# Optimization experiments

Hardware: AMD Instinct MI355X
Metric: run time of the kernel (lower is better)

The kernel has to match this reference:

```python
import jax, jax.numpy as jnp
import numpy as np

B, T, I, H, O = 65536, 28, 28, 64, 10


def setup_inputs() -> dict:
    key = jax.random.key(0)
    ks = jax.random.split(key, 8)
    s = 1.0 / np.sqrt(H)
    return {
        "x": jax.random.normal(ks[0], (B, T, I), dtype=jnp.float32),
        # PyTorch LSTM params: gate order i, f, g, o stacked along first dim
        "W_ih": jax.random.uniform(ks[1], (4 * H, I), minval=-s, maxval=s, dtype=jnp.float32),
        "W_hh": jax.random.uniform(ks[2], (4 * H, H), minval=-s, maxval=s, dtype=jnp.float32),
        "b_ih": jax.random.uniform(ks[3], (4 * H,), minval=-s, maxval=s, dtype=jnp.float32),
        "b_hh": jax.random.uniform(ks[4], (4 * H,), minval=-s, maxval=s, dtype=jnp.float32),
        "W_out": jax.random.uniform(ks[5], (O, H), minval=-s, maxval=s, dtype=jnp.float32),
        "b_out": jax.random.uniform(ks[6], (O,), minval=-s, maxval=s, dtype=jnp.float32),
    }


def _lstm_last_h(x, W_ih, W_hh, b_ih, b_hh):
    # x: [B, T, I]; returns final hidden state h_T: [B, H]
    b = b_ih + b_hh
    # precompute input projections for all timesteps: [T, B, 4H]
    xg = jnp.einsum("bti,gi->tbg", x, W_ih) + b

    def step(carry, xg_t):
        h, c = carry
        gates = xg_t + h @ W_hh.T  # [B, 4H]
        i, f, g, o = jnp.split(gates, 4, axis=-1)
        i = jax.nn.sigmoid(i)
        f = jax.nn.sigmoid(f)
        g = jnp.tanh(g)
        o = jax.nn.sigmoid(o)
        c = f * c + i * g
        h = o * jnp.tanh(c)
        return (h, c), None

    h0 = jnp.zeros((x.shape[0], W_hh.shape[1]), dtype=x.dtype)
    (h, c), _ = jax.lax.scan(step, (h0, h0), xg)
    return h


def reference(x, W_ih, W_hh, b_ih, b_hh, W_out, b_out):
    h = _lstm_last_h(x, W_ih, W_hh, b_ih, b_hh)  # [B, H]
    return h @ W_out.T + b_out  # [B, O]
```

## Files before the change

### kernel.cpp

```cpp
#include <hip/hip_runtime.h>
#include <hip/hip_bf16.h>
#include <stdint.h>
#include <stddef.h>

#define T_STEPS 28
#define I_DIM 28
#define H_DIM 64
#define O_DIM 10
#define BT 32
#define NTHREADS 256

typedef short bf16x8  __attribute__((ext_vector_type(8)));
typedef float f32x4   __attribute__((ext_vector_type(4)));

#define KS (-1.4426950408889634f)
#define KG ( 2.8853900817779268f)

__device__ __forceinline__ short f2bf(float f){
    uint32_t u = __builtin_bit_cast(uint32_t, f);
    u = (u + 0x7fffu + ((u >> 16) & 1u)) >> 16;
    return (short)u;
}
__device__ __forceinline__ float bf2f(short v){
    return __builtin_bit_cast(float, (uint32_t)(uint16_t)v << 16);
}
__device__ __forceinline__ uint32_t pack_bf16x2(float lo, float hi){
    float2 p2; p2.x = lo; p2.y = hi;
    __hip_bfloat162 p = __float22bfloat162_rn(p2);
    uint32_t u;
    __builtin_memcpy(&u, &p, 4);
    return u;
}

#define X_OFF(b)  ((b) * 2560)
#define H_OFF(b)  (5120 + (b) * 4608)
#define SMEM_BYTES (16896 + 48)

__global__ __launch_bounds__(NTHREADS, 4)
void lstm_fused(const float* __restrict__ x,
                const float* __restrict__ W_ih,
                const float* __restrict__ W_hh,
                const float* __restrict__ b_ih,
                const float* __restrict__ b_hh,
                const float* __restrict__ W_out,
                const float* __restrict__ b_out,
                float* __restrict__ out)
{
    __shared__ alignas(16) unsigned char smem[SMEM_BYTES];
    float* wout_t = (float*)(smem + 14336);
    float* bout_s = (float*)(smem + 16896);

    const int tid    = threadIdx.x;
    const int w      = tid >> 6;
    const int jgroup = w;
    const int lane = tid & 63;
    const int col  = lane & 15;
    const int quad = lane >> 4;
    const int jcol = jgroup * 16 + col;
    const int b0   = blockIdx.x * BT;

    bf16x8 wih[4];
    bf16x8 whh[2][4];
    #pragma unroll
    for (int nt = 0; nt < 4; ++nt){
        const float sc = (nt == 2) ? KG : KS;
        const int n = nt * 64 + jgroup * 16 + col;
        #pragma unroll
        for (int j = 0; j < 8; ++j){
            const int k = quad * 8 + j;
            wih[nt][j] = (k < I_DIM) ? f2bf(sc * W_ih[n * I_DIM + k])
                       : (k == I_DIM) ? f2bf(sc * (b_ih[n] + b_hh[n]))
                       : (short)0;
        }
        #pragma unroll
        for (int s = 0; s < 2; ++s)
            #pragma unroll
            for (int j = 0; j < 8; ++j){
                const int k = s * 32 + quad * 8 + j;
                whh[s][nt][j] = f2bf(sc * W_hh[n * H_DIM + k]);
            }
    }
    const f32x4 z4 = {0.0f, 0.0f, 0.0f, 0.0f};

    for (int idx = tid; idx < H_DIM * O_DIM; idx += NTHREADS){
        const int j = idx / O_DIM;
        const int o = idx - j * O_DIM;
        wout_t[idx] = W_out[o * H_DIM + j];
    }
    if (tid < O_DIM) bout_s[tid] = b_out[tid];

    for (int idx = tid; idx < BT * 72; idx += NTHREADS)
        ((short*)(smem + H_OFF(0)))[idx] = 0;

    const int row = tid >> 3;
    const int seg = tid & 7;
    const float* pxs = x + (size_t)(b0 + row) * (T_STEPS * I_DIM) + seg * 4;

    float xa[4];
    #pragma unroll
    for (int u = 0; u < 4; ++u){
        const int c = seg * 4 + u;
        xa[u] = (c < I_DIM) ? pxs[u] : (c == I_DIM ? 1.0f : 0.0f);
    }
    pxs += I_DIM;

    float cst[2][4];
    #pragma unroll
    for (int m = 0; m < 2; ++m)
        #pragma unroll
        for (int r = 0; r < 4; ++r) cst[m][r] = 0.0f;

    for (int t = 0; t < T_STEPS; ++t){
        short (*xb)[40] = (short(*)[40])(smem + X_OFF(t & 1));
        {
            uint2 v;
            v.x = pack_bf16x2(xa[0], xa[1]);
            v.y = pack_bf16x2(xa[2], xa[3]);
            *(uint2*)&xb[row][seg * 4] = v;
        }
        __syncthreads();

        if (t < T_STEPS - 1){
            #pragma unroll
            for (int u = 0; u < 4; ++u)
                if (seg * 4 + u < I_DIM) xa[u] = pxs[u];
            pxs += I_DIM;
        }

        const short (*hr)[72] = (const short(*)[72])(smem + H_OFF(t & 1));
        short (*hw)[72]       = (short(*)[72])(smem + H_OFF((t + 1) & 1));

        #pragma unroll
        for (int m = 0; m < 2; ++m){
            const int mt = m;

            f32x4 acc[4];
            {
                bf16x8 a = *(const bf16x8*)&xb[mt * 16 + col][quad * 8];
                #pragma unroll
                for (int nt = 0; nt < 4; ++nt)
                    acc[nt] = __builtin_amdgcn_mfma_f32_16x16x32_bf16(a, wih[nt], z4, 0, 0, 0);
            }
            #pragma unroll
            for (int s = 0; s < 2; ++s){
                bf16x8 a = *(const bf16x8*)&hr[mt * 16 + col][s * 32 + quad * 8];
                #pragma unroll
                for (int nt = 0; nt < 4; ++nt)
                    acc[nt] = __builtin_amdgcn_mfma_f32_16x16x32_bf16(a, whh[s][nt], acc[nt], 0, 0, 0);
            }

            float hv[4];
            #pragma unroll
            for (int p = 0; p < 2; ++p){
                const int r0 = 2 * p, r1 = 2 * p + 1;
                const float dA0 = 1.0f + __builtin_amdgcn_exp2f(acc[0][r0]);
                const float dA1 = 1.0f + __builtin_amdgcn_exp2f(acc[0][r1]);
                const float dB0 = 1.0f + __builtin_amdgcn_exp2f(acc[1][r0]);
                const float dB1 = 1.0f + __builtin_amdgcn_exp2f(acc[1][r1]);
                const float R10 = __builtin_amdgcn_rcpf(dA0 * dB0);
                const float R11 = __builtin_amdgcn_rcpf(dA1 * dB1);
                const float iv0 = R10 * dB0, fv0 = R10 * dA0;
                const float iv1 = R11 * dB1, fv1 = R11 * dA1;
                const float dG0 = 1.0f + __builtin_amdgcn_exp2f(acc[2][r0]);
                const float dG1 = 1.0f + __builtin_amdgcn_exp2f(acc[2][r1]);
                const float dO0 = 1.0f + __builtin_amdgcn_exp2f(acc[3][r0]);
                const float dO1 = 1.0f + __builtin_amdgcn_exp2f(acc[3][r1]);
                const float R20 = __builtin_amdgcn_rcpf(dG0 * dO0);
                const float R21 = __builtin_amdgcn_rcpf(dG1 * dO1);
                const float ov0 = R20 * dG0, ov1 = R21 * dG1;
                const float gv0 = 1.0f - 2.0f * (R20 * dO0);
                const float gv1 = 1.0f - 2.0f * (R21 * dO1);
                const float c0 = fv0 * cst[m][r0] + iv0 * gv0;
                const float c1 = fv1 * cst[m][r1] + iv1 * gv1;
                cst[m][r0] = c0; cst[m][r1] = c1;
                const float d50 = 1.0f + __builtin_amdgcn_exp2f(KG * c0);
                const float d51 = 1.0f + __builtin_amdgcn_exp2f(KG * c1);
                const float R5 = __builtin_amdgcn_rcpf(d50 * d51);
                const float t2 = 2.0f * R5;
                hv[r0] = ov0 * (1.0f - t2 * d51);
                hv[r1] = ov1 * (1.0f - t2 * d50);
            }
            #pragma unroll
            for (int rp = 0; rp < 2; ++rp){
                uint32_t u = pack_bf16x2(hv[2 * rp], hv[2 * rp + 1]);
                hw[mt * 16 + quad * 4 + 2 * rp    ][jcol] = (short)(u & 0xffffu);
                hw[mt * 16 + quad * 4 + 2 * rp + 1][jcol] = (short)(u >> 16);
            }
        }
    }
    __syncthreads();

    const short (*hfin)[72] = (const short(*)[72])(smem + H_OFF(0));
    for (int idx = tid; idx < BT * O_DIM; idx += NTHREADS){
        const int m = idx / O_DIM;
        const int o = idx - m * O_DIM;
        float s = bout_s[o];
        #pragma unroll 8
        for (int j = 0; j < H_DIM; ++j)
            s += bf2f(hfin[m][j]) * wout_t[j * O_DIM + o];
        out[(size_t)b0 * O_DIM + idx] = s;
    }
}

extern "C" void kernel_launch(void* const* d_in, const int* in_sizes, int n_in,
                              void* d_out, int out_size, void* d_ws, size_t ws_size,
                              hipStream_t stream) {
    const float* x     = (const float*)d_in[0];
    const float* W_ih  = (const float*)d_in[1];
    const float* W_hh  = (const float*)d_in[2];
    const float* b_ih  = (const float*)d_in[3];
    const float* b_hh  = (const float*)d_in[4];
    const float* W_out = (const float*)d_in[5];
    const float* b_out = (const float*)d_in[6];
    float* out = (float*)d_out;

    const int grid = 65536 / BT;
    lstm_fused<<<grid, NTHREADS, 0, stream>>>(x, W_ih, W_hh, b_ih, b_hh, W_out, b_out, out);
}
```

Before: 373.3 us.

## Double batch tile to 64 rows per block and vectorize x loads

```diff
diff --git a/kernel.cpp b/kernel.cpp
--- a/kernel.cpp
+++ b/kernel.cpp
@@ -7,7 +7,7 @@
 #define I_DIM 28
 #define H_DIM 64
 #define O_DIM 10
-#define BT 32
+#define BT 64
 #define NTHREADS 256
 
 typedef short bf16x8  __attribute__((ext_vector_type(8)));
@@ -32,9 +32,9 @@
     return u;
 }
 
-#define X_OFF(b)  ((b) * 2560)
-#define H_OFF(b)  (5120 + (b) * 4608)
-#define SMEM_BYTES (16896 + 48)
+#define X_OFF(b)  ((b) * 5120)
+#define H_OFF(b)  (10240 + (b) * 9216)
+#define SMEM_BYTES (31232 + 48)
 
 __global__ __launch_bounds__(NTHREADS, 4)
 void lstm_fused(const float* __restrict__ x,
@@ -47,8 +47,8 @@
                 float* __restrict__ out)
 {
     __shared__ alignas(16) unsigned char smem[SMEM_BYTES];
-    float* wout_t = (float*)(smem + 14336);
-    float* bout_s = (float*)(smem + 16896);
+    float* wout_t = (float*)(smem + 28672);
+    float* bout_s = (float*)(smem + 31232);
 
     const int tid    = threadIdx.x;
     const int w      = tid >> 6;
@@ -94,44 +94,53 @@
 
     const int row = tid >> 3;
     const int seg = tid & 7;
-    const float* pxs = x + (size_t)(b0 + row) * (T_STEPS * I_DIM) + seg * 4;
-
-    float xa[4];
+    const float* pxs0 = x + (size_t)(b0 + row     ) * (T_STEPS * I_DIM) + seg * 4;
+    const float* pxs1 = x + (size_t)(b0 + row + 32) * (T_STEPS * I_DIM) + seg * 4;
+
+    float xa0[4], xa1[4];
+    if (seg < 7){
+        float4 v0 = *(const float4*)pxs0;
+        float4 v1 = *(const float4*)pxs1;
+        xa0[0]=v0.x; xa0[1]=v0.y; xa0[2]=v0.z; xa0[3]=v0.w;
+        xa1[0]=v1.x; xa1[1]=v1.y; xa1[2]=v1.z; xa1[3]=v1.w;
+    } else {
+        xa0[0]=1.0f; xa0[1]=0.0f; xa0[2]=0.0f; xa0[3]=0.0f;
+        xa1[0]=1.0f; xa1[1]=0.0f; xa1[2]=0.0f; xa1[3]=0.0f;
+    }
+    pxs0 += I_DIM; pxs1 += I_DIM;
+
+    float cst[4][4];
     #pragma unroll
-    for (int u = 0; u < 4; ++u){
-        const int c = seg * 4 + u;
-        xa[u] = (c < I_DIM) ? pxs[u] : (c == I_DIM ? 1.0f : 0.0f);
-    }
-    pxs += I_DIM;
-
-    float cst[2][4];
-    #pragma unroll
-    for (int m = 0; m < 2; ++m)
+    for (int m = 0; m < 4; ++m)
         #pragma unroll
         for (int r = 0; r < 4; ++r) cst[m][r] = 0.0f;
 
     for (int t = 0; t < T_STEPS; ++t){
         short (*xb)[40] = (short(*)[40])(smem + X_OFF(t & 1));
         {
-            uint2 v;
-            v.x = pack_bf16x2(xa[0], xa[1]);
-            v.y = pack_bf16x2(xa[2], xa[3]);
-            *(uint2*)&xb[row][seg * 4] = v;
+            uint2 v0, v1;
+            v0.x = pack_bf16x2(xa0[0], xa0[1]);
+            v0.y = pack_bf16x2(xa0[2], xa0[3]);
+            v1.x = pack_bf16x2(xa1[0], xa1[1]);
+            v1.y = pack_bf16x2(xa1[2], xa1[3]);
+            *(uint2*)&xb[row     ][seg * 4] = v0;
+            *(uint2*)&xb[row + 32][seg * 4] = v1;
         }
         __syncthreads();
 
-        if (t < T_STEPS - 1){
-            #pragma unroll
-            for (int u = 0; u < 4; ++u)
-                if (seg * 4 + u < I_DIM) xa[u] = pxs[u];
-            pxs += I_DIM;
+        if (t < T_STEPS - 1 && seg < 7){
+            float4 v0 = *(const float4*)pxs0;
+            float4 v1 = *(const float4*)pxs1;
+            xa0[0]=v0.x; xa0[1]=v0.y; xa0[2]=v0.z; xa0[3]=v0.w;
+            xa1[0]=v1.x; xa1[1]=v1.y; xa1[2]=v1.z; xa1[3]=v1.w;
+            pxs0 += I_DIM; pxs1 += I_DIM;
         }
 
         const short (*hr)[72] = (const short(*)[72])(smem + H_OFF(t & 1));
         short (*hw)[72]       = (short(*)[72])(smem + H_OFF((t + 1) & 1));
 
         #pragma unroll
-        for (int m = 0; m < 2; ++m){
+        for (int m = 0; m < 4; ++m){
             const int mt = m;
 
             f32x4 acc[4];
```

Result: slower. 386.2 us (+3.5%).

## Switch to one-wave blocks of 16 rows with register-held recurrent weights

Applied to the files above, without the earlier changes.

```diff
diff --git a/kernel.cpp b/kernel.cpp
--- a/kernel.cpp
+++ b/kernel.cpp
@@ -7,8 +7,8 @@
 #define I_DIM 28
 #define H_DIM 64
 #define O_DIM 10
-#define BT 32
-#define NTHREADS 256
+#define BT 16
+#define NTHREADS 64
 
 typedef short bf16x8  __attribute__((ext_vector_type(8)));
 typedef float f32x4   __attribute__((ext_vector_type(4)));
@@ -32,11 +32,11 @@
     return u;
 }
 
-#define X_OFF(b)  ((b) * 2560)
-#define H_OFF(b)  (5120 + (b) * 4608)
-#define SMEM_BYTES (16896 + 48)
+#define WIH_OFF 0
+#define H_OFF   16384
+#define SMEM_BYTES (16384 + 2304)
 
-__global__ __launch_bounds__(NTHREADS, 4)
+__global__ __launch_bounds__(NTHREADS, 2)
 void lstm_fused(const float* __restrict__ x,
                 const float* __restrict__ W_ih,
                 const float* __restrict__ W_hh,
@@ -47,108 +47,88 @@
                 float* __restrict__ out)
 {
     __shared__ alignas(16) unsigned char smem[SMEM_BYTES];
-    float* wout_t = (float*)(smem + 14336);
-    float* bout_s = (float*)(smem + 16896);
+    short* wihs = (short*)(smem + WIH_OFF);
+    short (*hbuf)[72] = (short(*)[72])(smem + H_OFF);
 
-    const int tid    = threadIdx.x;
-    const int w      = tid >> 6;
-    const int jgroup = w;
-    const int lane = tid & 63;
+    const int lane = threadIdx.x;
     const int col  = lane & 15;
     const int quad = lane >> 4;
-    const int jcol = jgroup * 16 + col;
     const int b0   = blockIdx.x * BT;
 
-    bf16x8 wih[4];
-    bf16x8 whh[2][4];
     #pragma unroll
-    for (int nt = 0; nt < 4; ++nt){
-        const float sc = (nt == 2) ? KG : KS;
-        const int n = nt * 64 + jgroup * 16 + col;
+    for (int tile = 0; tile < 16; ++tile){
+        const float sc = (tile >= 8 && tile < 12) ? KG : KS;
+        const int n = tile * 16 + col;
+        const float* wr = W_ih + n * I_DIM;
+        bf16x8 fv;
         #pragma unroll
         for (int j = 0; j < 8; ++j){
             const int k = quad * 8 + j;
-            wih[nt][j] = (k < I_DIM) ? f2bf(sc * W_ih[n * I_DIM + k])
-                       : (k == I_DIM) ? f2bf(sc * (b_ih[n] + b_hh[n]))
-                       : (short)0;
+            const float v = (k < I_DIM) ? wr[k]
+                          : (k == I_DIM) ? (b_ih[n] + b_hh[n])
+                          : 0.0f;
+            fv[j] = f2bf(sc * v);
         }
+        *(bf16x8*)&wihs[(tile * 64 + lane) * 8] = fv;
+    }
+
+    bf16x8 whh[16][2];
+    #pragma unroll
+    for (int tile = 0; tile < 16; ++tile){
+        const float sc = (tile >= 8 && tile < 12) ? KG : KS;
+        const int n = tile * 16 + col;
+        const float* wr = W_hh + n * H_DIM;
         #pragma unroll
-        for (int s = 0; s < 2; ++s)
+        for (int s = 0; s < 2; ++s){
+            bf16x8 fv;
             #pragma unroll
-            for (int j = 0; j < 8; ++j){
-                const int k = s * 32 + quad * 8 + j;
-                whh[s][nt][j] = f2bf(sc * W_hh[n * H_DIM + k]);
-            }
+            for (int j = 0; j < 8; ++j)
+                fv[j] = f2bf(sc * wr[s * 32 + quad * 8 + j]);
+            whh[tile][s] = fv;
+        }
     }
     const f32x4 z4 = {0.0f, 0.0f, 0.0f, 0.0f};
 
-    for (int idx = tid; idx < H_DIM * O_DIM; idx += NTHREADS){
-        const int j = idx / O_DIM;
-        const int o = idx - j * O_DIM;
-        wout_t[idx] = W_out[o * H_DIM + j];
-    }
-    if (tid < O_DIM) bout_s[tid] = b_out[tid];
+    const float* px = x + (size_t)(b0 + col) * (T_STEPS * I_DIM) + quad * 8;
+    float4 xva = *(const float4*)px;
+    float4 xvb;
+    if (quad < 3) xvb = *(const float4*)(px + 4);
+    else          { xvb.x = 1.0f; xvb.y = 0.0f; xvb.z = 0.0f; xvb.w = 0.0f; }
 
-    for (int idx = tid; idx < BT * 72; idx += NTHREADS)
-        ((short*)(smem + H_OFF(0)))[idx] = 0;
-
-    const int row = tid >> 3;
-    const int seg = tid & 7;
-    const float* pxs = x + (size_t)(b0 + row) * (T_STEPS * I_DIM) + seg * 4;
-
-    float xa[4];
+    bf16x8 ha{}, hb{};
+    float cst[4][4];
     #pragma unroll
-    for (int u = 0; u < 4; ++u){
-        const int c = seg * 4 + u;
-        xa[u] = (c < I_DIM) ? pxs[u] : (c == I_DIM ? 1.0f : 0.0f);
-    }
-    pxs += I_DIM;
-
-    float cst[2][4];
-    #pragma unroll
-    for (int m = 0; m < 2; ++m)
+    for (int g = 0; g < 4; ++g)
         #pragma unroll
-        for (int r = 0; r < 4; ++r) cst[m][r] = 0.0f;
+        for (int r = 0; r < 4; ++r) cst[g][r] = 0.0f;
 
     for (int t = 0; t < T_STEPS; ++t){
-        short (*xb)[40] = (short(*)[40])(smem + X_OFF(t & 1));
-        {
-            uint2 v;
-            v.x = pack_bf16x2(xa[0], xa[1]);
-            v.y = pack_bf16x2(xa[2], xa[3]);
-            *(uint2*)&xb[row][seg * 4] = v;
-        }
-        __syncthreads();
+        uint4 uu;
+        uu.x = pack_bf16x2(xva.x, xva.y);
+        uu.y = pack_bf16x2(xva.z, xva.w);
+        uu.z = pack_bf16x2(xvb.x, xvb.y);
+        uu.w = pack_bf16x2(xvb.z, xvb.w);
+        bf16x8 xf; __builtin_memcpy(&xf, &uu, 16);
 
         if (t < T_STEPS - 1){
-            #pragma unroll
-            for (int u = 0; u < 4; ++u)
-                if (seg * 4 + u < I_DIM) xa[u] = pxs[u];
-            pxs += I_DIM;
+            px += I_DIM;
+            xva = *(const float4*)px;
+            if (quad < 3) xvb = *(const float4*)(px + 4);
         }
 
-        const short (*hr)[72] = (const short(*)[72])(smem + H_OFF(t & 1));
-        short (*hw)[72]       = (short(*)[72])(smem + H_OFF((t + 1) & 1));
-
         #pragma unroll
-        for (int m = 0; m < 2; ++m){
-            const int mt = m;
-
+        for (int g = 0; g < 4; ++g){
             f32x4 acc[4];
-            {
-                bf16x8 a = *(const bf16x8*)&xb[mt * 16 + col][quad * 8];
-                #pragma unroll
-                for (int nt = 0; nt < 4; ++nt)
-                    acc[nt] = __builtin_amdgcn_mfma_f32_16x16x32_bf16(a, wih[nt], z4, 0, 0, 0);
+            #pragma unroll
+            for (int gi = 0; gi < 4; ++gi){
+                const int tile = gi * 4 + g;
+                bf16x8 wf;
+                __builtin_memcpy(&wf, &wihs[(tile * 64 + lane) * 8], 16);
+                f32x4 a = __builtin_amdgcn_mfma_f32_16x16x32_bf16(xf, wf, z4, 0, 0, 0);
+                a = __builtin_amdgcn_mfma_f32_16x16x32_bf16(ha, whh[tile][0], a, 0, 0, 0);
+                a = __builtin_amdgcn_mfma_f32_16x16x32_bf16(hb, whh[tile][1], a, 0, 0, 0);
+                acc[gi] = a;
             }
-            #pragma unroll
-            for (int s = 0; s < 2; ++s){
-                bf16x8 a = *(const bf16x8*)&hr[mt * 16 + col][s * 32 + quad * 8];
-                #pragma unroll
-                for (int nt = 0; nt < 4; ++nt)
-                    acc[nt] = __builtin_amdgcn_mfma_f32_16x16x32_bf16(a, whh[s][nt], acc[nt], 0, 0, 0);
-            }
-
             float hv[4];
             #pragma unroll
             for (int p = 0; p < 2; ++p){
@@ -170,9 +150,9 @@
                 const float ov0 = R20 * dG0, ov1 = R21 * dG1;
                 const float gv0 = 1.0f - 2.0f * (R20 * dO0);
                 const float gv1 = 1.0f - 2.0f * (R21 * dO1);
-                const float c0 = fv0 * cst[m][r0] + iv0 * gv0;
-                const float c1 = fv1 * cst[m][r1] + iv1 * gv1;
-                cst[m][r0] = c0; cst[m][r1] = c1;
+                const float c0 = fv0 * cst[g][r0] + iv0 * gv0;
+                const float c1 = fv1 * cst[g][r1] + iv1 * gv1;
+                cst[g][r0] = c0; cst[g][r1] = c1;
                 const float d50 = 1.0f + __builtin_amdgcn_exp2f(KG * c0);
                 const float d51 = 1.0f + __builtin_amdgcn_exp2f(KG * c1);
                 const float R5 = __builtin_amdgcn_rcpf(d50 * d51);
@@ -182,22 +162,22 @@
             }
             #pragma unroll
             for (int rp = 0; rp < 2; ++rp){
-                uint32_t u = pack_bf16x2(hv[2 * rp], hv[2 * rp + 1]);
-                hw[mt * 16 + quad * 4 + 2 * rp    ][jcol] = (short)(u & 0xffffu);
-                hw[mt * 16 + quad * 4 + 2 * rp + 1][jcol] = (short)(u >> 16);
+                const uint32_t u2 = pack_bf16x2(hv[2 * rp], hv[2 * rp + 1]);
+                hbuf[4 * quad + 2 * rp    ][16 * g + col] = (short)(u2 & 0xffffu);
+                hbuf[4 * quad + 2 * rp + 1][16 * g + col] = (short)(u2 >> 16);
             }
         }
+        __builtin_memcpy(&ha, &hbuf[col][quad * 8],      16);
+        __builtin_memcpy(&hb, &hbuf[col][32 + quad * 8], 16);
     }
-    __syncthreads();
 
-    const short (*hfin)[72] = (const short(*)[72])(smem + H_OFF(0));
-    for (int idx = tid; idx < BT * O_DIM; idx += NTHREADS){
+    for (int idx = lane; idx < BT * O_DIM; idx += NTHREADS){
         const int m = idx / O_DIM;
         const int o = idx - m * O_DIM;
-        float s = bout_s[o];
+        float s = b_out[o];
         #pragma unroll 8
         for (int j = 0; j < H_DIM; ++j)
-            s += bf2f(hfin[m][j]) * wout_t[j * O_DIM + o];
+            s += bf2f(hbuf[m][j]) * W_out[o * H_DIM + j];
         out[(size_t)b0 * O_DIM + idx] = s;
     }
 }
```

After: 511.9 us. +37.1%, slower.
